# Optimization experiments

Measured on AMD Instinct MI355X. Metric: run time of the kernel, lower is better.

Reference implementation:

```python
import jax, jax.numpy as jnp
import numpy as np

B, C, H, W = 8, 512, 32, 32
NH = 8


def setup_inputs() -> dict:
    key = jax.random.key(0)
    ks = jax.random.split(key, 10)
    s = 1.0 / np.sqrt(C)
    return {
        "query": jax.random.normal(ks[0], (B, C, H, W), jnp.float32),
        "key": jax.random.normal(ks[1], (B, C, H, W), jnp.float32),
        "Wq": jax.random.normal(ks[2], (C, C), jnp.float32) * s,
        "bq": jnp.zeros((C,), jnp.float32),
        "Wk": jax.random.normal(ks[3], (C, C), jnp.float32) * s,
        "bk": jnp.zeros((C,), jnp.float32),
        "Wv": jax.random.normal(ks[4], (C, C), jnp.float32) * s,
        "bv": jnp.zeros((C,), jnp.float32),
        "Wo": jax.random.normal(ks[5], (C, C), jnp.float32) * s,
        "bo": jnp.zeros((C,), jnp.float32),
        "num_heads": NH,
    }


def reference(query, key, Wq, bq, Wk, bk, Wv, bv, Wo, bo, num_heads):
    b, c, h, w = query.shape
    hd = c // num_heads
    scale = hd ** (-0.5)
    # [B,C,H,W] -> [B, L, C] with L = H*W
    qf = jnp.transpose(query, (0, 2, 3, 1)).reshape(b, -1, c)
    kf = jnp.transpose(key, (0, 2, 3, 1)).reshape(b, -1, c)
    L = qf.shape[1]
    # Linear projections (torch Linear: x @ W.T + b); value = key
    q = qf @ Wq.T + bq
    k = kf @ Wk.T + bk
    v = kf @ Wv.T + bv
    # split heads: [B, L, NH, hd] -> [B, NH, L, hd]
    q = q.reshape(b, L, num_heads, hd).transpose(0, 2, 1, 3) * scale
    k = k.reshape(b, L, num_heads, hd).transpose(0, 2, 1, 3)
    v = v.reshape(b, L, num_heads, hd).transpose(0, 2, 1, 3)
    scores = jnp.einsum('bhqd,bhkd->bhqk', q, k)
    attn = jax.nn.softmax(scores, axis=-1)  # dropout p=0.0 -> identity
    o = jnp.einsum('bhqk,bhkd->bhqd', attn, v)
    o = o.transpose(0, 2, 1, 3).reshape(b, L, c)
    o = o @ Wo.T + bo
    o = o + qf + kf  # residual with flattened query and key
    return jnp.transpose(o.reshape(b, h, w, c), (0, 3, 1, 2))
```

## Files before the change

kernel.cpp:

```cpp
#include <hip/hip_runtime.h>
#include <stdint.h>

#define B_  8
#define C_  512
#define L_  1024
#define NH_ 8
#define HD_ 64

typedef __attribute__((ext_vector_type(8))) short short8;
typedef __attribute__((ext_vector_type(4))) short short4v;
typedef __attribute__((ext_vector_type(4))) float f32x4;
typedef __attribute__((ext_vector_type(2))) unsigned uint2v;

#define MFMA(a,b,c) __builtin_amdgcn_mfma_f32_16x16x32_bf16((a),(b),(c),0,0,0)
#define GLD16(g,l) __builtin_amdgcn_global_load_lds( \
    (const __attribute__((address_space(1))) void*)(g), \
    (__attribute__((address_space(3))) void*)(l), 16, 0, 0)

__device__ __forceinline__ unsigned short f2bf(float f) {
  union { float f; unsigned u; } x; x.f = f;
  unsigned r = x.u + 0x7FFFu + ((x.u >> 16) & 1u);
  return (unsigned short)(r >> 16);
}

__device__ __forceinline__ unsigned cvtpk_bf16(float lo, float hi) {
  unsigned r;
  asm("v_cvt_pk_bf16_f32 %0, %1, %2" : "=v"(r) : "v"(lo), "v"(hi));
  return r;
}

__global__ __launch_bounds__(256) void k_transpose(
    const float* __restrict__ q, const float* __restrict__ k,
    unsigned short* __restrict__ qf, unsigned short* __restrict__ kf,
    const float* __restrict__ w0, const float* __restrict__ w1,
    const float* __restrict__ w2, const float* __restrict__ w3,
    unsigned short* __restrict__ wdst) {
  const int z = blockIdx.z;
  if (z == 16) {
    const int gb = blockIdx.y * 32 + blockIdx.x;
    const float* s = (gb < 128) ? w0 : (gb < 256) ? w1 : (gb < 384) ? w2 : w3;
    const int off = (gb & 127) * 2048 + threadIdx.x * 8;
    float4 v0 = *(const float4*)&s[off];
    float4 v1 = *(const float4*)&s[off + 4];
    short8 p;
    p[0] = (short)f2bf(v0.x); p[1] = (short)f2bf(v0.y);
    p[2] = (short)f2bf(v0.z); p[3] = (short)f2bf(v0.w);
    p[4] = (short)f2bf(v1.x); p[5] = (short)f2bf(v1.y);
    p[6] = (short)f2bf(v1.z); p[7] = (short)f2bf(v1.w);
    *(short8*)&wdst[(size_t)(gb >> 7) * 262144 + off] = p;
    return;
  }
  __shared__ float t[32][33];
  const int b = z >> 1;
  const float* src = (z & 1) ? k : q;
  unsigned short* dst = (z & 1) ? kf : qf;
  const int tx = threadIdx.x & 31;
  const int ty = threadIdx.x >> 5;
  const int l0 = blockIdx.x * 32;
  const int c0 = blockIdx.y * 32;
#pragma unroll
  for (int i = 0; i < 4; ++i)
    t[ty + 8*i][tx] = src[((size_t)b * C_ + c0 + ty + 8*i) * L_ + l0 + tx];
  __syncthreads();
#pragma unroll
  for (int i = 0; i < 4; ++i)
    dst[((size_t)b * L_ + l0 + ty + 8*i) * C_ + c0 + tx] = f2bf(t[tx][ty + 8*i]);
}

template<int MREP>
__device__ __forceinline__ void gemm_core(
    const unsigned short* __restrict__ A, const unsigned short* __restrict__ W,
    const float* __restrict__ bias, void* __restrict__ outp,
    const float* __restrict__ resQ, const float* __restrict__ resK,
    int mode, float scale, unsigned short* lA, unsigned short* lB,
    int tm, int tn) {
  const int lane = threadIdx.x & 63;
  const int wid  = threadIdx.x >> 6;
  const int wm = wid >> 1, wn = wid & 1;
  const int r16 = lane & 15;
  const int g4  = lane >> 4;

  constexpr int ASLOTS = MREP * 128;
  constexpr int BSLOTS = 512;

  const int sB0 = wid * 128 + lane;
  const int rB0 = sB0 >> 2;
  const int cB0 = (sB0 & 3) ^ ((rB0 >> 1) & 3);
  const int sA0 = wid * (ASLOTS / 4) + lane;
  const int rA0 = sA0 >> 2;
  const int cA0 = (sA0 & 3) ^ ((rA0 >> 1) & 3);

#define G_STAGE(bb, kt) { \
    if constexpr (MREP == 4) { \
      GLD16(A + (size_t)(tm + rA0) * C_ + (kt) + cA0 * 8, &lA[(bb)*ASLOTS*8 + (wid*128)*8]); \
      GLD16(A + (size_t)(tm + rA0 + 16) * C_ + (kt) + cA0 * 8, &lA[(bb)*ASLOTS*8 + (wid*128+64)*8]); \
    } else { \
      GLD16(A + (size_t)(tm + rA0) * C_ + (kt) + cA0 * 8, &lA[(bb)*ASLOTS*8 + (wid*64)*8]); \
    } \
    GLD16(W + (size_t)(tn + rB0) * C_ + (kt) + cB0 * 8, &lB[(bb)*BSLOTS*8 + (wid*128)*8]); \
    GLD16(W + (size_t)(tn + rB0 + 16) * C_ + (kt) + cB0 * 8, &lB[(bb)*BSLOTS*8 + (wid*128+64)*8]); \
  }

  f32x4 acc[MREP][4];
#pragma unroll
  for (int i = 0; i < MREP; ++i)
#pragma unroll
    for (int j = 0; j < 4; ++j) acc[i][j] = (f32x4){0.f, 0.f, 0.f, 0.f};

  G_STAGE(0, 0);
  __syncthreads();

  int cur = 0;
  for (int t = 0; t < 16; ++t) {
    if (t < 15) G_STAGE(cur ^ 1, (t + 1) * 32);

    const unsigned short* cAb = &lA[cur * ASLOTS * 8];
    const unsigned short* cBb = &lB[cur * BSLOTS * 8];
    short8 af[MREP], bw[4];
#pragma unroll
    for (int i = 0; i < MREP; ++i) {
      int row = wm * (MREP * 16) + i * 16 + r16;
      af[i] = *(const short8*)&cAb[(row * 4 + (g4 ^ ((row >> 1) & 3))) * 8];
    }
#pragma unroll
    for (int j = 0; j < 4; ++j) {
      int row = wn * 64 + j * 16 + r16;
      bw[j] = *(const short8*)&cBb[(row * 4 + (g4 ^ ((row >> 1) & 3))) * 8];
    }
    __builtin_amdgcn_s_setprio(1);
#pragma unroll
    for (int i = 0; i < MREP; ++i)
#pragma unroll
      for (int j = 0; j < 4; ++j) acc[i][j] = MFMA(af[i], bw[j], acc[i][j]);
    __builtin_amdgcn_s_setprio(0);

    __syncthreads();
    cur ^= 1;
  }
#undef G_STAGE

  if (mode <= 1) {
    unsigned short* out = (unsigned short*)outp;
#pragma unroll
    for (int i = 0; i < MREP; ++i)
#pragma unroll
      for (int j = 0; j < 4; ++j) {
        int c = tn + wn*64 + j*16 + r16;
        float bia = bias[c];
        int h = c >> 6, d = c & 63;
#pragma unroll
        for (int r = 0; r < 4; ++r) {
          int gm = tm + wm*(MREP*16) + i*16 + g4*4 + r;
          int b = gm >> 10, l = gm & 1023;
          out[(((size_t)b * NH_ + h) * L_ + l) * HD_ + d] = f2bf((acc[i][j][r] + bia) * scale);
        }
      }
  } else if (mode == 2) {
    unsigned short* out = (unsigned short*)outp;
#pragma unroll
    for (int i = 0; i < MREP; ++i)
#pragma unroll
      for (int j = 0; j < 4; ++j) {
        int c = tn + wn*64 + j*16 + r16;
        float bia = bias[c];
        int h = c >> 6, d = c & 63;
        int gm0 = tm + wm*(MREP*16) + i*16 + g4*4;
        int b = gm0 >> 10, l0 = gm0 & 1023;
        short4v pk;
#pragma unroll
        for (int r = 0; r < 4; ++r) pk[r] = (short)f2bf(acc[i][j][r] + bia);
        *(short4v*)&out[(((size_t)b * NH_ + h) * HD_ + d) * L_ + l0] = pk;
      }
  } else {
    float* out = (float*)outp;
#pragma unroll
    for (int i = 0; i < MREP; ++i)
#pragma unroll
      for (int j = 0; j < 4; ++j) {
        int c = tn + wn*64 + j*16 + r16;
        float bia = bias[c];
        int gm0 = tm + wm*(MREP*16) + i*16 + g4*4;
        int b = gm0 >> 10, l0 = gm0 & 1023;
        size_t idx = ((size_t)b * C_ + c) * L_ + l0;
        float4 q4 = *(const float4*)&resQ[idx];
        float4 k4 = *(const float4*)&resK[idx];
        float4 o4;
        o4.x = acc[i][j][0] + bia + q4.x + k4.x;
        o4.y = acc[i][j][1] + bia + q4.y + k4.y;
        o4.z = acc[i][j][2] + bia + q4.z + k4.z;
        o4.w = acc[i][j][3] + bia + q4.w + k4.w;
        *(float4*)&out[idx] = o4;
      }
  }
}

__global__ __launch_bounds__(256) void k_proj(
    const unsigned short* __restrict__ qf, const unsigned short* __restrict__ kf,
    const unsigned short* __restrict__ Wqb, const unsigned short* __restrict__ Wkb,
    const unsigned short* __restrict__ Wvb,
    const float* __restrict__ bq, const float* __restrict__ bk, const float* __restrict__ bv,
    unsigned short* __restrict__ Qw, unsigned short* __restrict__ Kw,
    unsigned short* __restrict__ VTw) {
  __shared__ unsigned short lA[2 * 512 * 8];
  __shared__ unsigned short lB[2 * 512 * 8];
  const int bid = blockIdx.x;
  const int xcd = bid & 7;
  const int i_  = bid >> 3;
  const int ml  = i_ / 12;
  const int rem = i_ - ml * 12;
  const int z   = rem >> 2;
  const int n   = rem & 3;
  const int m   = xcd * 8 + ml;
  const unsigned short* A = (z == 0) ? qf : kf;
  const unsigned short* W = (z == 0) ? Wqb : (z == 1) ? Wkb : Wvb;
  const float* bias = (z == 0) ? bq : (z == 1) ? bk : bv;
  void* out = (z == 0) ? (void*)Qw : (z == 1) ? (void*)Kw : (void*)VTw;
  float scale = (z == 0) ? 0.125f * 1.44269504088896f : 1.0f;
  gemm_core<4>(A, W, bias, out, nullptr, nullptr, z, scale, lA, lB, m * 128, n * 128);
}

__global__ __launch_bounds__(256) void k_outproj(
    const unsigned short* __restrict__ O, const unsigned short* __restrict__ Wob,
    const float* __restrict__ bo, float* __restrict__ out,
    const float* __restrict__ query, const float* __restrict__ key) {
  __shared__ unsigned short lA[2 * 256 * 8];
  __shared__ unsigned short lB[2 * 512 * 8];
  const int bid = blockIdx.x;
  const int xcd = bid & 7;
  const int i_  = bid >> 3;
  const int m   = xcd * 16 + (i_ >> 2);
  const int n   = i_ & 3;
  gemm_core<2>(O, Wob, bo, out, query, key, 3, 1.0f, lA, lB, m * 64, n * 128);
}

__global__ __launch_bounds__(256, 2) void k_attn(
    const unsigned short* __restrict__ Q, const unsigned short* __restrict__ K,
    const unsigned short* __restrict__ VT, unsigned short* __restrict__ O) {
  __shared__ unsigned short Kt[2][64 * 64];
  __shared__ unsigned short Vt[2][64 * 64];
  const int lane = threadIdx.x & 63;
  const int wid  = threadIdx.x >> 6;
  const int bid  = blockIdx.x;
  const int xcd  = bid & 7;
  const int i_   = bid >> 3;
  const int bh   = xcd * 8 + (i_ >> 3);
  const int qb   = i_ & 7;
  const int qrow0 = qb * 128 + wid * 32;
  const int r16 = lane & 15;
  const int g4  = lane >> 4;
  const size_t base = (size_t)bh * L_ * HD_;
  const unsigned short* Kg = K + base;
  const unsigned short* Vg = VT + base;

  const int s0 = wid * 128 + lane;
  const int row0 = s0 >> 3;
  const int row1 = (s0 + 64) >> 3;
  const int chK0 = (s0 & 7) ^ ((row0 >> 1) & 7);
  const int chK1 = ((s0 + 64) & 7) ^ ((row1 >> 1) & 7);
  const int chV0 = (s0 & 7) ^ (row0 & 7);
  const int chV1 = ((s0 + 64) & 7) ^ (row1 & 7);

#define STAGE_KV(nxt, kt0) { \
    GLD16(Kg + (size_t)((kt0) + row0) * HD_ + chK0 * 8, &Kt[nxt][(wid*128)*8]); \
    GLD16(Kg + (size_t)((kt0) + row1) * HD_ + chK1 * 8, &Kt[nxt][(wid*128+64)*8]); \
    GLD16(Vg + (size_t)row0 * L_ + (kt0) + chV0 * 8, &Vt[nxt][(wid*128)*8]); \
    GLD16(Vg + (size_t)row1 * L_ + (kt0) + chV1 * 8, &Vt[nxt][(wid*128+64)*8]); \
  }

  short8 qv[2][2];
#pragma unroll
  for (int i = 0; i < 2; ++i)
#pragma unroll
    for (int ks = 0; ks < 2; ++ks)
      qv[i][ks] = *(const short8*)(Q + base + (size_t)(qrow0 + i*16 + r16) * HD_ + ks*32 + g4*8);

  short8 vones;
#pragma unroll
  for (int e = 0; e < 8; ++e) vones[e] = (short)0x3F80;

  f32x4 lacc[2];
  f32x4 oacc[2][4];
#pragma unroll
  for (int i = 0; i < 2; ++i) {
    lacc[i] = (f32x4){0.f, 0.f, 0.f, 0.f};
#pragma unroll
    for (int j = 0; j < 4; ++j) oacc[i][j] = (f32x4){0.f, 0.f, 0.f, 0.f};
  }

  STAGE_KV(0, 0);
  __syncthreads();

  const int sK = (4 * (r16 >> 2) + (r16 & 3)) & 7;
  const int swz = r16 & 7;

  int cur = 0;
  for (int t = 0; t < 16; ++t) {
    if (t < 15) STAGE_KV(cur ^ 1, (t + 1) * 64);

    const unsigned short* lK = &Kt[cur][0];
    const unsigned short* lV = &Vt[cur][0];

    f32x4 sc[2][4];
#pragma unroll
    for (int i = 0; i < 2; ++i)
#pragma unroll
      for (int cf = 0; cf < 4; ++cf) sc[i][cf] = (f32x4){0.f, 0.f, 0.f, 0.f};

    __builtin_amdgcn_s_setprio(1);
#pragma unroll
    for (int cf = 0; cf < 4; ++cf) {
      const int h = cf >> 1, c = cf & 1;
      const int rr = h*32 + ((r16 >> 2) << 3) + ((r16 & 3) << 1) + c;
      const int rowb = rr * 64;
      short8 kb0 = *(const short8*)&lK[rowb + ((g4) ^ sK) * 8];
      short8 kb1 = *(const short8*)&lK[rowb + ((4 + g4) ^ sK) * 8];
      sc[0][cf] = MFMA(kb0, qv[0][0], sc[0][cf]);
      sc[0][cf] = MFMA(kb1, qv[0][1], sc[0][cf]);
      sc[1][cf] = MFMA(kb0, qv[1][0], sc[1][cf]);
      sc[1][cf] = MFMA(kb1, qv[1][1], sc[1][cf]);
    }
    __builtin_amdgcn_s_setprio(0);

#pragma unroll
    for (int h = 0; h < 2; ++h) {
      union { unsigned u[4]; short8 s8; } pu0, pu1;
#pragma unroll
      for (int r = 0; r < 4; ++r) {
        pu0.u[r] = cvtpk_bf16(exp2f(sc[0][h*2][r]), exp2f(sc[0][h*2+1][r]));
        pu1.u[r] = cvtpk_bf16(exp2f(sc[1][h*2][r]), exp2f(sc[1][h*2+1][r]));
      }
      short8 pa0 = pu0.s8;
      short8 pa1 = pu1.s8;
      __builtin_amdgcn_s_setprio(1);
      lacc[0] = MFMA(pa0, vones, lacc[0]);
      lacc[1] = MFMA(pa1, vones, lacc[1]);
#pragma unroll
      for (int j = 0; j < 4; ++j) {
        short8 vb = *(const short8*)&lV[(j*16 + r16) * 64 + ((h*4 + g4) ^ swz) * 8];
        oacc[0][j] = MFMA(pa0, vb, oacc[0][j]);
        oacc[1][j] = MFMA(pa1, vb, oacc[1][j]);
      }
      __builtin_amdgcn_s_setprio(0);
    }

    __syncthreads();
    cur ^= 1;
  }
#undef STAGE_KV

  const int b = bh >> 3, h = bh & 7;
#pragma unroll
  for (int i = 0; i < 2; ++i) {
    float linv[4];
#pragma unroll
    for (int r = 0; r < 4; ++r) linv[r] = 1.0f / lacc[i][r];
#pragma unroll
    for (int j = 0; j < 4; ++j)
#pragma unroll
      for (int r = 0; r < 4; ++r) {
        int row = qrow0 + i*16 + g4*4 + r;
        int col = h*64 + j*16 + r16;
        O[((size_t)b * L_ + row) * C_ + col] = f2bf(oacc[i][j][r] * linv[r]);
      }
  }
}

extern "C" void kernel_launch(void* const* d_in, const int* in_sizes, int n_in,
                              void* d_out, int out_size, void* d_ws, size_t ws_size,
                              hipStream_t stream) {
  (void)in_sizes; (void)n_in; (void)out_size; (void)ws_size;
  const float* query = (const float*)d_in[0];
  const float* key   = (const float*)d_in[1];
  const float* Wq = (const float*)d_in[2];
  const float* bq = (const float*)d_in[3];
  const float* Wk = (const float*)d_in[4];
  const float* bk = (const float*)d_in[5];
  const float* Wv = (const float*)d_in[6];
  const float* bv = (const float*)d_in[7];
  const float* Wo = (const float*)d_in[8];
  const float* bo = (const float*)d_in[9];

  char* ws = (char*)d_ws;
  unsigned short* qf  = (unsigned short*)(ws);
  unsigned short* kf  = (unsigned short*)(ws + 8388608);
  unsigned short* Wqb = (unsigned short*)(ws + 16777216);
  unsigned short* Wkb = Wqb + 262144;
  unsigned short* Wvb = Wkb + 262144;
  unsigned short* Wob = Wvb + 262144;
  unsigned short* Qw  = (unsigned short*)(ws + 18874368);
  unsigned short* Kw  = (unsigned short*)(ws + 27262976);
  unsigned short* VTw = (unsigned short*)(ws + 35651584);
  unsigned short* Ow  = (unsigned short*)(ws + 44040192);

  k_transpose<<<dim3(32, 16, 17), 256, 0, stream>>>(query, key, qf, kf,
                                                    Wq, Wk, Wv, Wo, Wqb);
  k_proj<<<dim3(768), 256, 0, stream>>>(qf, kf, Wqb, Wkb, Wvb, bq, bk, bv, Qw, Kw, VTw);
  k_attn<<<dim3(512), 256, 0, stream>>>(Qw, Kw, VTw, Ow);
  k_outproj<<<dim3(512), 256, 0, stream>>>(Ow, Wob, bo, (float*)d_out, query, key);
}
```

Baseline: 93.94 us.

## Fuse fp32 transpose and bf16 conversion into projection GEMM loads

Removes the separate transpose/convert kernel. The projection GEMM now reads fp32 NCHW activations and fp32 weights straight from global memory into registers, converts them to bf16, and writes them into swizzled LDS. The output projection likewise converts fp32 Wo on the fly. This drops a launch and a full bf16 intermediate round trip, at the cost of register-staged loads instead of async global-to-LDS copies and repeated per-block conversion of the weights.

```diff
diff --git a/kernel.cpp b/kernel.cpp
--- a/kernel.cpp
+++ b/kernel.cpp
@@ -29,76 +29,71 @@
   return r;
 }
 
-__global__ __launch_bounds__(256) void k_transpose(
-    const float* __restrict__ q, const float* __restrict__ k,
-    unsigned short* __restrict__ qf, unsigned short* __restrict__ kf,
-    const float* __restrict__ w0, const float* __restrict__ w1,
-    const float* __restrict__ w2, const float* __restrict__ w3,
-    unsigned short* __restrict__ wdst) {
-  const int z = blockIdx.z;
-  if (z == 16) {
-    const int gb = blockIdx.y * 32 + blockIdx.x;
-    const float* s = (gb < 128) ? w0 : (gb < 256) ? w1 : (gb < 384) ? w2 : w3;
-    const int off = (gb & 127) * 2048 + threadIdx.x * 8;
-    float4 v0 = *(const float4*)&s[off];
-    float4 v1 = *(const float4*)&s[off + 4];
-    short8 p;
-    p[0] = (short)f2bf(v0.x); p[1] = (short)f2bf(v0.y);
-    p[2] = (short)f2bf(v0.z); p[3] = (short)f2bf(v0.w);
-    p[4] = (short)f2bf(v1.x); p[5] = (short)f2bf(v1.y);
-    p[6] = (short)f2bf(v1.z); p[7] = (short)f2bf(v1.w);
-    *(short8*)&wdst[(size_t)(gb >> 7) * 262144 + off] = p;
-    return;
-  }
-  __shared__ float t[32][33];
-  const int b = z >> 1;
-  const float* src = (z & 1) ? k : q;
-  unsigned short* dst = (z & 1) ? kf : qf;
-  const int tx = threadIdx.x & 31;
-  const int ty = threadIdx.x >> 5;
-  const int l0 = blockIdx.x * 32;
-  const int c0 = blockIdx.y * 32;
-#pragma unroll
-  for (int i = 0; i < 4; ++i)
-    t[ty + 8*i][tx] = src[((size_t)b * C_ + c0 + ty + 8*i) * L_ + l0 + tx];
-  __syncthreads();
-#pragma unroll
-  for (int i = 0; i < 4; ++i)
-    dst[((size_t)b * L_ + l0 + ty + 8*i) * C_ + c0 + tx] = f2bf(t[tx][ty + 8*i]);
-}
-
-template<int MREP>
+template<int MREP, int AF32>
 __device__ __forceinline__ void gemm_core(
-    const unsigned short* __restrict__ A, const unsigned short* __restrict__ W,
+    const float* __restrict__ Af32, const unsigned short* __restrict__ Abf,
+    const float* __restrict__ Wf,
     const float* __restrict__ bias, void* __restrict__ outp,
     const float* __restrict__ resQ, const float* __restrict__ resK,
     int mode, float scale, unsigned short* lA, unsigned short* lB,
     int tm, int tn) {
-  const int lane = threadIdx.x & 63;
-  const int wid  = threadIdx.x >> 6;
+  const int tid  = threadIdx.x;
+  const int lane = tid & 63;
+  const int wid  = tid >> 6;
   const int wm = wid >> 1, wn = wid & 1;
   const int r16 = lane & 15;
   const int g4  = lane >> 4;
 
-  constexpr int ASLOTS = MREP * 128;
-  constexpr int BSLOTS = 512;
-
-  const int sB0 = wid * 128 + lane;
-  const int rB0 = sB0 >> 2;
-  const int cB0 = (sB0 & 3) ^ ((rB0 >> 1) & 3);
-  const int sA0 = wid * (ASLOTS / 4) + lane;
-  const int rA0 = sA0 >> 2;
-  const int cA0 = (sA0 & 3) ^ ((rA0 >> 1) & 3);
-
-#define G_STAGE(bb, kt) { \
-    if constexpr (MREP == 4) { \
-      GLD16(A + (size_t)(tm + rA0) * C_ + (kt) + cA0 * 8, &lA[(bb)*ASLOTS*8 + (wid*128)*8]); \
-      GLD16(A + (size_t)(tm + rA0 + 16) * C_ + (kt) + cA0 * 8, &lA[(bb)*ASLOTS*8 + (wid*128+64)*8]); \
-    } else { \
-      GLD16(A + (size_t)(tm + rA0) * C_ + (kt) + cA0 * 8, &lA[(bb)*ASLOTS*8 + (wid*64)*8]); \
+  constexpr int ASHORTS = MREP * 1024;
+  constexpr int BSHORTS = 4096;
+
+  const int aL  = tid & 127;
+  const int aKg = tid >> 7;
+  const int gRow = tid >> 2, gCh = tid & 3;
+  const int bN0 = tid >> 3;
+  const int bK4 = tid & 7;
+
+  float areg[4][4], breg[4][4];
+
+#define LOADS(kt) { \
+    if constexpr (AF32) { \
+      _Pragma("unroll") \
+      for (int g = 0; g < 4; ++g) { \
+        const int q = aKg + g*2; \
+        _Pragma("unroll") \
+        for (int i = 0; i < 4; ++i) \
+          areg[g][i] = Af32[(size_t)((kt) + q*4 + i) * 1024 + aL]; \
+      } \
     } \
-    GLD16(W + (size_t)(tn + rB0) * C_ + (kt) + cB0 * 8, &lB[(bb)*BSLOTS*8 + (wid*128)*8]); \
-    GLD16(W + (size_t)(tn + rB0 + 16) * C_ + (kt) + cB0 * 8, &lB[(bb)*BSLOTS*8 + (wid*128+64)*8]); \
+    _Pragma("unroll") \
+    for (int g = 0; g < 4; ++g) { \
+      const int n = bN0 + g*32; \
+      float4 ld = *(const float4*)&Wf[(size_t)(tn + n) * 512 + (kt) + bK4*4]; \
+      breg[g][0] = ld.x; breg[g][1] = ld.y; breg[g][2] = ld.z; breg[g][3] = ld.w; \
+    } \
+  }
+
+#define WRITES(bb) { \
+    if constexpr (AF32) { \
+      _Pragma("unroll") \
+      for (int g = 0; g < 4; ++g) { \
+        const int q = aKg + g*2; \
+        const int pq = (q + 2*((aL>>1)&3)) & 7; \
+        uint2v w; \
+        w[0] = cvtpk_bf16(areg[g][0], areg[g][1]); \
+        w[1] = cvtpk_bf16(areg[g][2], areg[g][3]); \
+        *(uint2v*)&lA[(bb)*ASHORTS + aL*32 + pq*4] = w; \
+      } \
+    } \
+    _Pragma("unroll") \
+    for (int g = 0; g < 4; ++g) { \
+      const int n = bN0 + g*32; \
+      const int pq = (bK4 + 2*((n>>1)&3)) & 7; \
+      uint2v w; \
+      w[0] = cvtpk_bf16(breg[g][0], breg[g][1]); \
+      w[1] = cvtpk_bf16(breg[g][2], breg[g][3]); \
+      *(uint2v*)&lB[(bb)*BSHORTS + n*32 + pq*4] = w; \
+    } \
   }
 
   f32x4 acc[MREP][4];
@@ -107,25 +102,36 @@
 #pragma unroll
     for (int j = 0; j < 4; ++j) acc[i][j] = (f32x4){0.f, 0.f, 0.f, 0.f};
 
-  G_STAGE(0, 0);
+  LOADS(0);
+  if constexpr (!AF32)
+    GLD16(Abf + (size_t)(tm + gRow) * C_ + gCh * 8, &lA[0] + (size_t)0 + (tid * 8));
+  WRITES(0);
   __syncthreads();
 
   int cur = 0;
   for (int t = 0; t < 16; ++t) {
-    if (t < 15) G_STAGE(cur ^ 1, (t + 1) * 32);
-
-    const unsigned short* cAb = &lA[cur * ASLOTS * 8];
-    const unsigned short* cBb = &lB[cur * BSLOTS * 8];
+    const int kt1 = (t + 1) * 32;
+    if (t < 15) {
+      LOADS(kt1);
+      if constexpr (!AF32)
+        GLD16(Abf + (size_t)(tm + gRow) * C_ + kt1 + gCh * 8,
+              &lA[(cur ^ 1) * ASHORTS] + (tid * 8));
+    }
+
+    const unsigned short* cAb = &lA[cur * ASHORTS];
+    const unsigned short* cBb = &lB[cur * BSHORTS];
     short8 af[MREP], bw[4];
 #pragma unroll
     for (int i = 0; i < MREP; ++i) {
-      int row = wm * (MREP * 16) + i * 16 + r16;
-      af[i] = *(const short8*)&cAb[(row * 4 + (g4 ^ ((row >> 1) & 3))) * 8];
+      const int row = wm * (MREP * 16) + i * 16 + r16;
+      const int ch = AF32 ? ((g4 + (row >> 1)) & 3) : g4;
+      af[i] = *(const short8*)&cAb[row * 32 + ch * 8];
     }
 #pragma unroll
     for (int j = 0; j < 4; ++j) {
-      int row = wn * 64 + j * 16 + r16;
-      bw[j] = *(const short8*)&cBb[(row * 4 + (g4 ^ ((row >> 1) & 3))) * 8];
+      const int row = wn * 64 + j * 16 + r16;
+      const int ch = (g4 + (row >> 1)) & 3;
+      bw[j] = *(const short8*)&cBb[row * 32 + ch * 8];
     }
     __builtin_amdgcn_s_setprio(1);
 #pragma unroll
@@ -134,10 +140,12 @@
       for (int j = 0; j < 4; ++j) acc[i][j] = MFMA(af[i], bw[j], acc[i][j]);
     __builtin_amdgcn_s_setprio(0);
 
+    if (t < 15) WRITES(cur ^ 1);
     __syncthreads();
     cur ^= 1;
   }
-#undef G_STAGE
+#undef LOADS
+#undef WRITES
 
   if (mode <= 1) {
     unsigned short* out = (unsigned short*)outp;
@@ -195,14 +203,14 @@
 }
 
 __global__ __launch_bounds__(256) void k_proj(
-    const unsigned short* __restrict__ qf, const unsigned short* __restrict__ kf,
-    const unsigned short* __restrict__ Wqb, const unsigned short* __restrict__ Wkb,
-    const unsigned short* __restrict__ Wvb,
+    const float* __restrict__ query, const float* __restrict__ key,
+    const float* __restrict__ Wq, const float* __restrict__ Wk,
+    const float* __restrict__ Wv,
     const float* __restrict__ bq, const float* __restrict__ bk, const float* __restrict__ bv,
     unsigned short* __restrict__ Qw, unsigned short* __restrict__ Kw,
     unsigned short* __restrict__ VTw) {
-  __shared__ unsigned short lA[2 * 512 * 8];
-  __shared__ unsigned short lB[2 * 512 * 8];
+  __shared__ unsigned short lA[2 * 4096];
+  __shared__ unsigned short lB[2 * 4096];
   const int bid = blockIdx.x;
   const int xcd = bid & 7;
   const int i_  = bid >> 3;
@@ -211,26 +219,30 @@
   const int z   = rem >> 2;
   const int n   = rem & 3;
   const int m   = xcd * 8 + ml;
-  const unsigned short* A = (z == 0) ? qf : kf;
-  const unsigned short* W = (z == 0) ? Wqb : (z == 1) ? Wkb : Wvb;
+  const int tm = m * 128;
+  const int bBatch = tm >> 10, l0 = tm & 1023;
+  const float* Asrc = ((z == 0) ? query : key) + (size_t)bBatch * 512 * 1024 + l0;
+  const float* W = (z == 0) ? Wq : (z == 1) ? Wk : Wv;
   const float* bias = (z == 0) ? bq : (z == 1) ? bk : bv;
   void* out = (z == 0) ? (void*)Qw : (z == 1) ? (void*)Kw : (void*)VTw;
   float scale = (z == 0) ? 0.125f * 1.44269504088896f : 1.0f;
-  gemm_core<4>(A, W, bias, out, nullptr, nullptr, z, scale, lA, lB, m * 128, n * 128);
+  gemm_core<4, 1>(Asrc, nullptr, W, bias, out, nullptr, nullptr, z, scale,
+                  lA, lB, tm, n * 128);
 }
 
 __global__ __launch_bounds__(256) void k_outproj(
-    const unsigned short* __restrict__ O, const unsigned short* __restrict__ Wob,
+    const unsigned short* __restrict__ O, const float* __restrict__ Wo,
     const float* __restrict__ bo, float* __restrict__ out,
     const float* __restrict__ query, const float* __restrict__ key) {
-  __shared__ unsigned short lA[2 * 256 * 8];
-  __shared__ unsigned short lB[2 * 512 * 8];
+  __shared__ unsigned short lA[2 * 2048];
+  __shared__ unsigned short lB[2 * 4096];
   const int bid = blockIdx.x;
   const int xcd = bid & 7;
   const int i_  = bid >> 3;
   const int m   = xcd * 16 + (i_ >> 2);
   const int n   = i_ & 3;
-  gemm_core<2>(O, Wob, bo, out, query, key, 3, 1.0f, lA, lB, m * 64, n * 128);
+  gemm_core<2, 0>(nullptr, O, Wo, bo, out, query, key, 3, 1.0f,
+                  lA, lB, m * 64, n * 128);
 }
 
 __global__ __launch_bounds__(256, 2) void k_attn(
@@ -381,20 +393,13 @@
   const float* bo = (const float*)d_in[9];
 
   char* ws = (char*)d_ws;
-  unsigned short* qf  = (unsigned short*)(ws);
-  unsigned short* kf  = (unsigned short*)(ws + 8388608);
-  unsigned short* Wqb = (unsigned short*)(ws + 16777216);
-  unsigned short* Wkb = Wqb + 262144;
-  unsigned short* Wvb = Wkb + 262144;
-  unsigned short* Wob = Wvb + 262144;
   unsigned short* Qw  = (unsigned short*)(ws + 18874368);
   unsigned short* Kw  = (unsigned short*)(ws + 27262976);
   unsigned short* VTw = (unsigned short*)(ws + 35651584);
   unsigned short* Ow  = (unsigned short*)(ws + 44040192);
 
-  k_transpose<<<dim3(32, 16, 17), 256, 0, stream>>>(query, key, qf, kf,
-                                                    Wq, Wk, Wv, Wo, Wqb);
-  k_proj<<<dim3(768), 256, 0, stream>>>(qf, kf, Wqb, Wkb, Wvb, bq, bk, bv, Qw, Kw, VTw);
+  k_proj<<<dim3(768), 256, 0, stream>>>(query, key, Wq, Wk, Wv,
+                                        bq, bk, bv, Qw, Kw, VTw);
   k_attn<<<dim3(512), 256, 0, stream>>>(Qw, Kw, VTw, Ow);
-  k_outproj<<<dim3(512), 256, 0, stream>>>(Ow, Wob, bo, (float*)d_out, query, key);
-}
+  k_outproj<<<dim3(512), 256, 0, stream>>>(Ow, Wo, bo, (float*)d_out, query, key);
+}
```

New measurement: 99.02 us. 5.4% more time.

## Switch GEMM and attention K/V staging to triple-buffered prefetch with one barrier

Applied to the files above, without the earlier changes.

Moves the projection GEMMs and the attention kernel from double to triple buffering in LDS. Tiles are prefetched two iterations ahead, and a vmcnt wait counts only the outstanding loads of the older stage, so each iteration needs a single barrier instead of two. This is meant to hide global-to-LDS latency and reduce barrier stalls. The cost is more LDS per block, and attention launch bounds rise to 3 blocks per SM, which may constrain registers. The hand-written vmcnt counts must match the number of loads issued per stage.

```diff
diff --git a/kernel.cpp b/kernel.cpp
--- a/kernel.cpp
+++ b/kernel.cpp
@@ -108,11 +108,23 @@
     for (int j = 0; j < 4; ++j) acc[i][j] = (f32x4){0.f, 0.f, 0.f, 0.f};
 
   G_STAGE(0, 0);
-  __syncthreads();
+  G_STAGE(1, 32);
 
   int cur = 0;
+#pragma unroll 1
   for (int t = 0; t < 16; ++t) {
-    if (t < 15) G_STAGE(cur ^ 1, (t + 1) * 32);
+    if (t < 15) {
+      if constexpr (MREP == 4) asm volatile("s_waitcnt vmcnt(4)" ::: "memory");
+      else                     asm volatile("s_waitcnt vmcnt(3)" ::: "memory");
+    } else {
+      asm volatile("s_waitcnt vmcnt(0)" ::: "memory");
+    }
+    __builtin_amdgcn_s_barrier();
+    __builtin_amdgcn_sched_barrier(0);
+    if (t < 14) {
+      int nb = cur + 2; if (nb >= 3) nb -= 3;
+      G_STAGE(nb, (t + 2) * 32);
+    }
 
     const unsigned short* cAb = &lA[cur * ASLOTS * 8];
     const unsigned short* cBb = &lB[cur * BSLOTS * 8];
@@ -134,8 +146,7 @@
       for (int j = 0; j < 4; ++j) acc[i][j] = MFMA(af[i], bw[j], acc[i][j]);
     __builtin_amdgcn_s_setprio(0);
 
-    __syncthreads();
-    cur ^= 1;
+    cur = (cur + 1 == 3) ? 0 : cur + 1;
   }
 #undef G_STAGE
 
@@ -201,8 +212,8 @@
     const float* __restrict__ bq, const float* __restrict__ bk, const float* __restrict__ bv,
     unsigned short* __restrict__ Qw, unsigned short* __restrict__ Kw,
     unsigned short* __restrict__ VTw) {
-  __shared__ unsigned short lA[2 * 512 * 8];
-  __shared__ unsigned short lB[2 * 512 * 8];
+  __shared__ unsigned short lA[3 * 512 * 8];
+  __shared__ unsigned short lB[3 * 512 * 8];
   const int bid = blockIdx.x;
   const int xcd = bid & 7;
   const int i_  = bid >> 3;
@@ -223,8 +234,8 @@
     const unsigned short* __restrict__ O, const unsigned short* __restrict__ Wob,
     const float* __restrict__ bo, float* __restrict__ out,
     const float* __restrict__ query, const float* __restrict__ key) {
-  __shared__ unsigned short lA[2 * 256 * 8];
-  __shared__ unsigned short lB[2 * 512 * 8];
+  __shared__ unsigned short lA[3 * 256 * 8];
+  __shared__ unsigned short lB[3 * 512 * 8];
   const int bid = blockIdx.x;
   const int xcd = bid & 7;
   const int i_  = bid >> 3;
@@ -233,11 +244,11 @@
   gemm_core<2>(O, Wob, bo, out, query, key, 3, 1.0f, lA, lB, m * 64, n * 128);
 }
 
-__global__ __launch_bounds__(256, 2) void k_attn(
+__global__ __launch_bounds__(256, 3) void k_attn(
     const unsigned short* __restrict__ Q, const unsigned short* __restrict__ K,
     const unsigned short* __restrict__ VT, unsigned short* __restrict__ O) {
-  __shared__ unsigned short Kt[2][64 * 64];
-  __shared__ unsigned short Vt[2][64 * 64];
+  __shared__ unsigned short Kt[3][64 * 64];
+  __shared__ unsigned short Vt[3][64 * 64];
   const int lane = threadIdx.x & 63;
   const int wid  = threadIdx.x >> 6;
   const int bid  = blockIdx.x;
@@ -288,14 +299,22 @@
   }
 
   STAGE_KV(0, 0);
-  __syncthreads();
+  STAGE_KV(1, 64);
 
   const int sK = (4 * (r16 >> 2) + (r16 & 3)) & 7;
   const int swz = r16 & 7;
 
   int cur = 0;
+#pragma unroll 1
   for (int t = 0; t < 16; ++t) {
-    if (t < 15) STAGE_KV(cur ^ 1, (t + 1) * 64);
+    if (t < 15) asm volatile("s_waitcnt vmcnt(4)" ::: "memory");
+    else        asm volatile("s_waitcnt vmcnt(0)" ::: "memory");
+    __builtin_amdgcn_s_barrier();
+    __builtin_amdgcn_sched_barrier(0);
+    if (t < 14) {
+      int nb = cur + 2; if (nb >= 3) nb -= 3;
+      STAGE_KV(nb, (t + 2) * 64);
+    }
 
     const unsigned short* lK = &Kt[cur][0];
     const unsigned short* lV = &Vt[cur][0];
@@ -343,8 +362,7 @@
       __builtin_amdgcn_s_setprio(0);
     }
 
-    __syncthreads();
-    cur ^= 1;
+    cur = (cur + 1 == 3) ? 0 : cur + 1;
   }
 #undef STAGE_KV
 
```

After: 95.40 us. No clear change (+1.6%).
